# Optimization experiments

Measured on AMD Instinct MI355X. Metric: run time of the kernel, lower is better.

The kernel has to match this reference:

```python
import jax, jax.numpy as jnp
import numpy as np

DEPTH, DIM, HEADS, DH, MLP = 2, 512, 8, 64, 2048
INNER = HEADS * DH
B, L = 2, 2048
SCALE = DH ** -0.5
LN_EPS = 1e-5


def setup_inputs() -> dict:
    key = jax.random.key(0)
    ks = jax.random.split(key, 8)
    s = 0.02
    return {
        "x": jax.random.normal(ks[0], (B, L, DIM), dtype=jnp.float32),
        "mask": jax.random.randint(ks[1], (B, L, L), 0, 2, dtype=jnp.int32),
        "ln1_g": jnp.ones((DEPTH, DIM), jnp.float32),
        "ln1_b": jnp.zeros((DEPTH, DIM), jnp.float32),
        "w_qkv": jax.random.normal(ks[2], (DEPTH, DIM, 3 * INNER), jnp.float32) * s,
        "w_out": jax.random.normal(ks[3], (DEPTH, INNER, DIM), jnp.float32) * s,
        "b_out": jnp.zeros((DEPTH, DIM), jnp.float32),
        "ln2_g": jnp.ones((DEPTH, DIM), jnp.float32),
        "ln2_b": jnp.zeros((DEPTH, DIM), jnp.float32),
        "w1": jax.random.normal(ks[4], (DEPTH, DIM, MLP), jnp.float32) * s,
        "b1": jnp.zeros((DEPTH, MLP), jnp.float32),
        "w2": jax.random.normal(ks[5], (DEPTH, MLP, DIM), jnp.float32) * s,
        "b2": jnp.zeros((DEPTH, DIM), jnp.float32),
    }


def _layer_norm(x, g, b):
    m = jnp.mean(x, axis=-1, keepdims=True)
    v = jnp.mean(jnp.square(x - m), axis=-1, keepdims=True)
    return (x - m) * jax.lax.rsqrt(v + LN_EPS) * g + b


def _attention(h, mask_f, w_qkv, w_out, b_out):
    b, l, _ = h.shape
    qkv = h @ w_qkv  # [b,l,3*inner]
    qkv = qkv.reshape(b, l, 3, HEADS, DH)
    q = jnp.transpose(qkv[:, :, 0], (0, 2, 1, 3))  # [b,h,l,dh]
    k = jnp.transpose(qkv[:, :, 1], (0, 2, 1, 3))
    v = jnp.transpose(qkv[:, :, 2], (0, 2, 1, 3))
    scores = jnp.einsum('bhqd,bhkd->bhqk', q, k) * SCALE
    attn = jax.nn.softmax(scores, axis=-1)
    # multiplicative mask + renormalization (non-standard)
    attn = attn * mask_f
    attn = attn / (jnp.sum(attn, axis=-1, keepdims=True) + 1e-10)
    z = jnp.einsum('bhqk,bhkd->bhqd', attn, v)
    z = jnp.transpose(z, (0, 2, 1, 3)).reshape(b, l, INNER)
    return z @ w_out + b_out


def reference(x, mask, ln1_g, ln1_b, w_qkv, w_out, b_out, ln2_g, ln2_b, w1, b1, w2, b2):
    mask_f = mask[:, None, :, :].astype(x.dtype)  # [b,1,l,l]
    h = x
    for d in range(DEPTH):
        a = _attention(_layer_norm(h, ln1_g[d], ln1_b[d]), mask_f,
                       w_qkv[d], w_out[d], b_out[d])
        h = h + a
        f = _layer_norm(h, ln2_g[d], ln2_b[d])
        f = jax.nn.gelu(f @ w1[d] + b1[d], approximate=False) @ w2[d] + b2[d]
        h = h + f
    return h
```

## Files before the change

### kernel.cpp

```cpp
#include <hip/hip_runtime.h>
#include <math.h>

#define DEPTH 2
#define DIM   512
#define HEADS 8
#define DH    64
#define INNER 512
#define MLP_D 2048
#define BSZ   2
#define SEQ   2048
#define MROWS (BSZ*SEQ)
#define SCALE 0.125f
#define QSC   0.18033688f
#define LN_EPS 1e-5f

typedef unsigned short u16;
typedef unsigned int   u32;
typedef __attribute__((ext_vector_type(8))) unsigned short u16x8;
typedef __attribute__((ext_vector_type(4))) unsigned short u16x4;
typedef __attribute__((ext_vector_type(8))) short          s16x8;
typedef __attribute__((ext_vector_type(4))) float          f32x4;

__device__ __forceinline__ u16 f2bf(float f) {
    u32 u = __float_as_uint(f);
    u += 0x7fffu + ((u >> 16) & 1u);
    return (u16)(u >> 16);
}
__device__ __forceinline__ u32 cvtpk(float lo, float hi) {
    u32 r;
    asm("v_cvt_pk_bf16_f32 %0, %1, %2" : "=v"(r) : "v"(lo), "v"(hi));
    return r;
}
__device__ __forceinline__ void gld16(const void* g, void* l) {
    __builtin_amdgcn_global_load_lds(
        (const __attribute__((address_space(1))) void*)g,
        (__attribute__((address_space(3))) void*)l, 16, 0, 0);
}

__device__ __forceinline__ float wred_sum(float v) {
    #pragma unroll
    for (int o = 32; o; o >>= 1) v += __shfl_xor(v, o);
    return v;
}

__global__ __launch_bounds__(256) void ln_kernel(
    const float* __restrict__ x, const float* __restrict__ g,
    const float* __restrict__ b, u16* __restrict__ y)
{
    const int wave = threadIdx.x >> 6;
    const int lane = threadIdx.x & 63;
    const int row  = blockIdx.x * 4 + wave;
    const float* xr = x + (size_t)row * DIM;

    float4 v0 = *reinterpret_cast<const float4*>(&xr[lane * 8]);
    float4 v1 = *reinterpret_cast<const float4*>(&xr[lane * 8 + 4]);

    float s = v0.x + v0.y + v0.z + v0.w + v1.x + v1.y + v1.z + v1.w;
    s = wred_sum(s);
    const float mean = s * (1.0f / DIM);

    float d[8] = {v0.x - mean, v0.y - mean, v0.z - mean, v0.w - mean,
                  v1.x - mean, v1.y - mean, v1.z - mean, v1.w - mean};
    float ss = 0.f;
    #pragma unroll
    for (int i = 0; i < 8; ++i) ss += d[i] * d[i];
    ss = wred_sum(ss);
    const float inv = rsqrtf(ss * (1.0f / DIM) + LN_EPS);

    float4 g0 = *reinterpret_cast<const float4*>(&g[lane * 8]);
    float4 g1 = *reinterpret_cast<const float4*>(&g[lane * 8 + 4]);
    float4 b0 = *reinterpret_cast<const float4*>(&b[lane * 8]);
    float4 b1 = *reinterpret_cast<const float4*>(&b[lane * 8 + 4]);
    const float gg[8] = {g0.x, g0.y, g0.z, g0.w, g1.x, g1.y, g1.z, g1.w};
    const float bb[8] = {b0.x, b0.y, b0.z, b0.w, b1.x, b1.y, b1.z, b1.w};

    u16x8 o;
    #pragma unroll
    for (int i = 0; i < 8; ++i) o[i] = f2bf(d[i] * inv * gg[i] + bb[i]);
    *reinterpret_cast<u16x8*>(&y[(size_t)row * DIM + lane * 8]) = o;
}

__global__ __launch_bounds__(256) void transpose_bf16_kernel(
    const float* __restrict__ in, u16* __restrict__ out, int K, int N)
{
    __shared__ u16 t[64][65];
    const int k0 = blockIdx.y * 64, n0 = blockIdx.x * 64;
    const int tid = threadIdx.x;
    #pragma unroll
    for (int i = 0; i < 4; ++i) {
        int idx = tid + i * 256;
        int r = idx >> 4, c4 = idx & 15;
        float4 v = *reinterpret_cast<const float4*>(&in[(size_t)(k0 + r) * N + n0 + c4 * 4]);
        t[c4 * 4 + 0][r] = f2bf(v.x);
        t[c4 * 4 + 1][r] = f2bf(v.y);
        t[c4 * 4 + 2][r] = f2bf(v.z);
        t[c4 * 4 + 3][r] = f2bf(v.w);
    }
    __syncthreads();
    #pragma unroll
    for (int i = 0; i < 2; ++i) {
        int idx = tid + i * 256;
        int r = idx >> 3, c8 = idx & 7;
        u16x8 w;
        #pragma unroll
        for (int j = 0; j < 8; ++j) w[j] = t[r][c8 * 8 + j];
        *reinterpret_cast<u16x8*>(&out[(size_t)(n0 + r) * K + k0 + c8 * 8]) = w;
    }
}

__global__ __launch_bounds__(256) void mask_pack_kernel(
    const int* __restrict__ mask, u32* __restrict__ mbT)
{
    const int wv = threadIdx.x >> 6, lane = threadIdx.x & 63;
    const int row = blockIdx.x * 4 + wv;
    const int b = row >> 11, l = row & (SEQ - 1);
    const int* mr = mask + (size_t)row * SEQ;
    u32* out = mbT + (size_t)b * 64 * SEQ;
    for (int it = 0; it < 32; ++it) {
        unsigned long long bal = __ballot(mr[it * 64 + lane] != 0);
        if (lane == 0) {
            out[(size_t)(2 * it) * SEQ + l]     = (u32)bal;
            out[(size_t)(2 * it + 1) * SEQ + l] = (u32)(bal >> 32);
        }
    }
}

#define GSTAGE(buf, kt) do {                                                   \
    const int k0_ = (kt) * BK;                                                 \
    _Pragma("unroll")                                                          \
    for (int i_ = 0; i_ < ACH; ++i_) {                                         \
        int idx_ = i_ * 256 + tid; int r_ = idx_ >> 2, kc_ = idx_ & 3;         \
        gld16(&A[(size_t)(bm + r_) * K + k0_ + kc_ * 8],                       \
              &As[buf][(size_t)(i_ * 256 + (wid << 6)) * 8]);                  \
    }                                                                          \
    _Pragma("unroll")                                                          \
    for (int i_ = 0; i_ < BCH; ++i_) {                                         \
        int idx_ = i_ * 256 + tid; int r_ = idx_ >> 2, kc_ = idx_ & 3;         \
        gld16(&BT[(size_t)(bn + r_) * K + k0_ + kc_ * 8],                      \
              &Bs[buf][(size_t)(i_ * 256 + (wid << 6)) * 8]);                  \
    }                                                                          \
} while (0)

template<int BM, int BN, int MT, int NT, int EPI>
__global__ __launch_bounds__(256) void gemm_bf16(
    const u16* __restrict__ A, const u16* __restrict__ BT,
    const float* __restrict__ bias, const float* __restrict__ Cin,
    void* __restrict__ CoutV, u16* __restrict__ qo, u16* __restrict__ ko,
    u16* __restrict__ vo, int M, int N, int K)
{
    constexpr int BK = 32;
    constexpr int WC = BN / (NT * 16);
    constexpr int ACH = (BM * BK) / (256 * 8);
    constexpr int BCH = (BN * BK) / (256 * 8);

    __shared__ __align__(16) u16 As[2][BM * BK];
    __shared__ __align__(16) u16 Bs[2][BN * BK];

    const int tid  = threadIdx.x;
    const int lane = tid & 63, wid = tid >> 6;
    const int wr = wid / WC, wc = wid % WC;
    const int lr = lane & 15, lk = lane >> 4;
    const int bm = blockIdx.y * BM, bn = blockIdx.x * BN;

    f32x4 acc[MT][NT];
    #pragma unroll
    for (int i = 0; i < MT; ++i)
        #pragma unroll
        for (int j = 0; j < NT; ++j) {
            acc[i][j][0] = 0.f; acc[i][j][1] = 0.f;
            acc[i][j][2] = 0.f; acc[i][j][3] = 0.f;
        }

    GSTAGE(0, 0);
    asm volatile("s_waitcnt vmcnt(0)" ::: "memory");
    __syncthreads();

    const int NTILES = K / BK;
    int cur = 0;
    for (int t = 0; t < NTILES; ++t) {
        if (t + 1 < NTILES) GSTAGE(cur ^ 1, t + 1);

        s16x8 af[MT], bf[NT];
        #pragma unroll
        for (int mt = 0; mt < MT; ++mt)
            af[mt] = *reinterpret_cast<const s16x8*>(
                &As[cur][(wr * MT * 16 + mt * 16 + lr) * BK + lk * 8]);
        #pragma unroll
        for (int nt = 0; nt < NT; ++nt)
            bf[nt] = *reinterpret_cast<const s16x8*>(
                &Bs[cur][(wc * NT * 16 + nt * 16 + lr) * BK + lk * 8]);
        #pragma unroll
        for (int mt = 0; mt < MT; ++mt)
            #pragma unroll
            for (int nt = 0; nt < NT; ++nt)
                acc[mt][nt] = __builtin_amdgcn_mfma_f32_16x16x32_bf16(
                    af[mt], bf[nt], acc[mt][nt], 0, 0, 0);

        asm volatile("s_waitcnt vmcnt(0)" ::: "memory");
        __syncthreads();
        cur ^= 1;
    }

    if (EPI == 3) {
        #pragma unroll
        for (int mt = 0; mt < MT; ++mt) {
            const int rbase = bm + wr * MT * 16 + mt * 16 + lk * 4;
            #pragma unroll
            for (int nt = 0; nt < NT; ++nt) {
                const int c = bn + wc * NT * 16 + nt * 16 + lr;
                const int sec = c >> 9, hh = (c >> 6) & 7, dd = c & 63;
                if (sec == 0) {
                    #pragma unroll
                    for (int i = 0; i < 4; ++i)
                        qo[((size_t)hh * MROWS + rbase + i) * 64 + dd] =
                            f2bf(acc[mt][nt][i] * QSC);
                } else if (sec == 1) {
                    #pragma unroll
                    for (int i = 0; i < 4; ++i)
                        ko[((size_t)hh * MROWS + rbase + i) * 64 + dd] =
                            f2bf(acc[mt][nt][i]);
                } else {
                    const int pos = (rbase & ~31) + lk * 8 + (mt & 1) * 4;
                    u16x4 o;
                    #pragma unroll
                    for (int i = 0; i < 4; ++i) o[i] = f2bf(acc[mt][nt][i]);
                    *reinterpret_cast<u16x4*>(
                        &vo[((size_t)hh * 64 + dd) * MROWS + pos]) = o;
                }
            }
        }
        return;
    }
    #pragma unroll
    for (int mt = 0; mt < MT; ++mt) {
        #pragma unroll
        for (int i = 0; i < 4; ++i) {
            const size_t r = bm + wr * MT * 16 + mt * 16 + lk * 4 + i;
            #pragma unroll
            for (int nt = 0; nt < NT; ++nt) {
                const size_t c = bn + wc * NT * 16 + nt * 16 + lr;
                float v = acc[mt][nt][i];
                if (EPI == 1) {
                    v += bias[c];
                    v = 0.5f * v * (1.0f + erff(v * 0.70710678118654752f));
                    ((u16*)CoutV)[r * N + c] = f2bf(v);
                } else {
                    v += bias[c] + Cin[r * N + c];
                    ((float*)CoutV)[r * N + c] = v;
                }
            }
        }
    }
}
#undef GSTAGE

#define ASTAGE(buf, kv) do {                                                   \
    _Pragma("unroll")                                                          \
    for (int i_ = 0; i_ < 4; ++i_) {                                           \
        int idx_ = i_ * 256 + tid; int r_ = idx_ >> 3, c_ = idx_ & 7;          \
        gld16(Kbase + (size_t)((kv) + r_) * 64 + ((c_ ^ (r_ & 7)) * 8),        \
              &Ks[buf][(size_t)(i_ * 256 + (wid << 6)) * 8]);                  \
    }                                                                          \
    _Pragma("unroll")                                                          \
    for (int i_ = 0; i_ < 4; ++i_) {                                           \
        int idx_ = i_ * 256 + tid; int r_ = idx_ >> 4, c_ = idx_ & 15;         \
        gld16(Vbase + (size_t)r_ * MROWS + (kv) + ((c_ ^ (r_ & 7)) * 8),       \
              &Vts[buf][(size_t)(i_ * 256 + (wid << 6)) * 8]);                 \
    }                                                                          \
} while (0)

__global__ __launch_bounds__(256) void attn_mfma_kernel(
    const u16* __restrict__ Qb,
    const u16* __restrict__ Kb,
    const u16* __restrict__ Vtb,
    const u32* __restrict__ mbT,
    u16* __restrict__ z)
{
    const int bh = blockIdx.y;
    const int b = bh >> 3, h = bh & 7;
    const int q0 = blockIdx.x * 64;
    const int tid = threadIdx.x;
    const int wid = tid >> 6, lane = tid & 63;
    const int lr = lane & 15, lk = lane >> 4;
    const int lr7 = lr & 7;

    __shared__ __align__(16) u16 Ks[2][128 * 64];
    __shared__ __align__(16) u16 Vts[2][64 * 128];

    const int qrow = q0 + wid * 16 + lr;
    const size_t qg = (size_t)b * SEQ + qrow;

    s16x8 qf0, qf1;
    {
        const u16* Qrow = Qb + ((size_t)h * MROWS + qg) * 64;
        qf0 = *reinterpret_cast<const s16x8*>(Qrow + lk * 8);
        qf1 = *reinterpret_cast<const s16x8*>(Qrow + 32 + lk * 8);
    }

    float Mx = -1e30f, Sm = 0.f;
    f32x4 zacc[4];
    #pragma unroll
    for (int dt = 0; dt < 4; ++dt) {
        zacc[dt][0] = 0.f; zacc[dt][1] = 0.f; zacc[dt][2] = 0.f; zacc[dt][3] = 0.f;
    }

    const u16* Kbase = Kb + ((size_t)h * MROWS + (size_t)b * SEQ) * 64;
    const u16* Vbase = Vtb + (size_t)h * 64 * MROWS + (size_t)b * SEQ;
    const u32* mbase = mbT + (size_t)b * 64 * SEQ;

    ASTAGE(0, 0);
    asm volatile("s_waitcnt vmcnt(0)" ::: "memory");
    __syncthreads();

    int cur = 0;
    for (int t = 0; t < SEQ / 128; ++t) {
        if (t + 1 < SEQ / 128) ASTAGE(cur ^ 1, (t + 1) * 128);

        u32 mw[4];
        #pragma unroll
        for (int j = 0; j < 4; ++j)
            mw[j] = mbase[(size_t)(t * 4 + j) * SEQ + qrow];

        const u16* Kc = Ks[cur];
        f32x4 st[8];
        #pragma unroll
        for (int mt = 0; mt < 8; ++mt) {
            st[mt][0] = 0.f; st[mt][1] = 0.f; st[mt][2] = 0.f; st[mt][3] = 0.f;
        }
        #pragma unroll
        for (int mt = 0; mt < 8; ++mt) {
            const s16x8 a0 = *reinterpret_cast<const s16x8*>(
                &Kc[(mt * 16 + lr) * 64 + ((lk ^ lr7) * 8)]);
            const s16x8 a1 = *reinterpret_cast<const s16x8*>(
                &Kc[(mt * 16 + lr) * 64 + (((lk + 4) ^ lr7) * 8)]);
            st[mt] = __builtin_amdgcn_mfma_f32_16x16x32_bf16(a0, qf0, st[mt], 0, 0, 0);
            st[mt] = __builtin_amdgcn_mfma_f32_16x16x32_bf16(a1, qf1, st[mt], 0, 0, 0);
        }

        float ml = st[0][0];
        #pragma unroll
        for (int mt = 0; mt < 8; ++mt)
            #pragma unroll
            for (int i = 0; i < 4; ++i) ml = fmaxf(ml, st[mt][i]);
        ml = fmaxf(ml, __shfl_xor(ml, 16));
        ml = fmaxf(ml, __shfl_xor(ml, 32));
        if (__any(ml > Mx + 8.f)) {
            const float Mn = fmaxf(Mx, ml);
            const float r  = exp2f(Mx - Mn);
            Sm *= r;
            #pragma unroll
            for (int dt = 0; dt < 4; ++dt)
                #pragma unroll
                for (int i = 0; i < 4; ++i) zacc[dt][i] *= r;
            Mx = Mn;
        }
        float tm = 0.f;
        #pragma unroll
        for (int mt = 0; mt < 8; ++mt) {
            const u32 wsh = mw[mt >> 1] >> (((mt & 1) << 4) | (lk << 2));
            #pragma unroll
            for (int i = 0; i < 4; ++i) {
                float e = exp2f(st[mt][i] - Mx);
                e = ((wsh >> i) & 1u) ? e : 0.f;
                st[mt][i] = e;
                tm += e;
            }
        }
        tm += __shfl_xor(tm, 16);
        tm += __shfl_xor(tm, 32);
        Sm += tm;

        const u16* Vc = Vts[cur];
        #pragma unroll
        for (int s = 0; s < 4; ++s) {
            union { u32 w[4]; s16x8 v; } pu;
            pu.w[0] = cvtpk(st[2 * s][0], st[2 * s][1]);
            pu.w[1] = cvtpk(st[2 * s][2], st[2 * s][3]);
            pu.w[2] = cvtpk(st[2 * s + 1][0], st[2 * s + 1][1]);
            pu.w[3] = cvtpk(st[2 * s + 1][2], st[2 * s + 1][3]);
            #pragma unroll
            for (int dt = 0; dt < 4; ++dt) {
                const s16x8 av = *reinterpret_cast<const s16x8*>(
                    &Vc[(dt * 16 + lr) * 128 + (((s * 4 + lk) ^ lr7) * 8)]);
                zacc[dt] = __builtin_amdgcn_mfma_f32_16x16x32_bf16(av, pu.v, zacc[dt], 0, 0, 0);
            }
        }

        asm volatile("s_waitcnt vmcnt(0)" ::: "memory");
        __syncthreads();
        cur ^= 1;
    }

    const float inv = 1.0f / (Sm + 1e-10f);
    #pragma unroll
    for (int dt = 0; dt < 4; ++dt) {
        u16x4 o;
        #pragma unroll
        for (int i = 0; i < 4; ++i) o[i] = f2bf(zacc[dt][i] * inv);
        *reinterpret_cast<u16x4*>(
            &z[qg * INNER + h * 64 + dt * 16 + lk * 4]) = o;
    }
}
#undef ASTAGE

extern "C" void kernel_launch(void* const* d_in, const int* in_sizes, int n_in,
                              void* d_out, int out_size, void* d_ws, size_t ws_size,
                              hipStream_t stream) {
    const float* x      = (const float*)d_in[0];
    const int*   mask   = (const int*)  d_in[1];
    const float* ln1_g  = (const float*)d_in[2];
    const float* ln1_b  = (const float*)d_in[3];
    const float* w_qkv  = (const float*)d_in[4];
    const float* w_out  = (const float*)d_in[5];
    const float* b_out  = (const float*)d_in[6];
    const float* ln2_g  = (const float*)d_in[7];
    const float* ln2_b  = (const float*)d_in[8];
    const float* w1     = (const float*)d_in[9];
    const float* b1     = (const float*)d_in[10];
    const float* w2     = (const float*)d_in[11];
    const float* b2     = (const float*)d_in[12];

    float* h = (float*)d_out;

    u16* hn  = (u16*)d_ws;
    u16* zb  = hn + (size_t)MROWS * DIM;
    u32* mbT = (u32*)(zb + (size_t)MROWS * DIM);
    u16* wT  = (u16*)(mbT + (size_t)BSZ * 64 * SEQ);
    const size_t WT_LAYER = (size_t)DIM * 3 * INNER + (size_t)INNER * DIM
                          + (size_t)DIM * MLP_D + (size_t)MLP_D * DIM;
    u16* big = wT + DEPTH * WT_LAYER;
    u16* Qb  = big;
    u16* Kb  = Qb + (size_t)HEADS * MROWS * 64;
    u16* Vtb = Kb + (size_t)HEADS * MROWS * 64;
    u16* f1  = big;

    hipMemcpyAsync(h, x, (size_t)MROWS * DIM * sizeof(float),
                   hipMemcpyDeviceToDevice, stream);

    mask_pack_kernel<<<MROWS / 4, 256, 0, stream>>>(mask, mbT);
    for (int d = 0; d < DEPTH; ++d) {
        u16* wqkvT = wT + d * WT_LAYER;
        u16* woutT = wqkvT + (size_t)3 * INNER * DIM;
        u16* w1T   = woutT + (size_t)DIM * INNER;
        u16* w2T   = w1T   + (size_t)MLP_D * DIM;
        transpose_bf16_kernel<<<dim3(3 * INNER / 64, DIM / 64), 256, 0, stream>>>(
            w_qkv + (size_t)d * DIM * 3 * INNER, wqkvT, DIM, 3 * INNER);
        transpose_bf16_kernel<<<dim3(INNER / 64, DIM / 64), 256, 0, stream>>>(
            w_out + (size_t)d * INNER * DIM, woutT, INNER, DIM);
        transpose_bf16_kernel<<<dim3(MLP_D / 64, DIM / 64), 256, 0, stream>>>(
            w1 + (size_t)d * DIM * MLP_D, w1T, DIM, MLP_D);
        transpose_bf16_kernel<<<dim3(DIM / 64, MLP_D / 64), 256, 0, stream>>>(
            w2 + (size_t)d * MLP_D * DIM, w2T, MLP_D, DIM);
    }

    for (int d = 0; d < DEPTH; ++d) {
        u16* wqkvT = wT + d * WT_LAYER;
        u16* woutT = wqkvT + (size_t)3 * INNER * DIM;
        u16* w1T   = woutT + (size_t)DIM * INNER;
        u16* w2T   = w1T   + (size_t)MLP_D * DIM;

        ln_kernel<<<MROWS / 4, 256, 0, stream>>>(h, ln1_g + d * DIM, ln1_b + d * DIM, hn);

        gemm_bf16<128, 128, 4, 4, 3><<<dim3(3 * INNER / 128, MROWS / 128), 256, 0, stream>>>(
            hn, wqkvT, nullptr, nullptr, nullptr, Qb, Kb, Vtb, MROWS, 3 * INNER, DIM);

        attn_mfma_kernel<<<dim3(SEQ / 64, BSZ * HEADS), 256, 0, stream>>>(
            Qb, Kb, Vtb, mbT, zb);

        gemm_bf16<128, 64, 4, 2, 2><<<dim3(DIM / 64, MROWS / 128), 256, 0, stream>>>(
            zb, woutT, b_out + d * DIM, h, h, nullptr, nullptr, nullptr, MROWS, DIM, INNER);

        ln_kernel<<<MROWS / 4, 256, 0, stream>>>(h, ln2_g + d * DIM, ln2_b + d * DIM, hn);

        gemm_bf16<128, 128, 4, 4, 1><<<dim3(MLP_D / 128, MROWS / 128), 256, 0, stream>>>(
            hn, w1T, b1 + d * MLP_D, nullptr, f1, nullptr, nullptr, nullptr, MROWS, MLP_D, DIM);

        gemm_bf16<128, 64, 4, 2, 2><<<dim3(DIM / 64, MROWS / 128), 256, 0, stream>>>(
            f1, w2T, b2 + d * DIM, h, h, nullptr, nullptr, nullptr, MROWS, DIM, MLP_D);
    }
}
```

Baseline: 439.6 us.

## Split attention KV across two wave groups, fuse weight transposes, shrink GEMM tiles

The attention kernel now runs 512 threads per block. Two groups of four waves each process half of the key/value sequence with separate LDS buffers, and their partial max, sum and output accumulators are merged through shared memory at the end. This doubles the wave parallelism per query tile on a grid that was small (512 blocks). All per-layer weight transpose launches are fused into one kernel, and the GEMM tile M is reduced from 128 to 64 to launch more blocks. The cost is an extra LDS merge step, half the waves idling during the final write, and less reuse per GEMM tile.

```diff
diff --git a/kernel.cpp b/kernel.cpp
--- a/kernel.cpp
+++ b/kernel.cpp
@@ -80,31 +80,60 @@
     *reinterpret_cast<u16x8*>(&y[(size_t)row * DIM + lane * 8]) = o;
 }
 
-__global__ __launch_bounds__(256) void transpose_bf16_kernel(
-    const float* __restrict__ in, u16* __restrict__ out, int K, int N)
+__global__ __launch_bounds__(256) void transpose_all_kernel(
+    const float* __restrict__ w_qkv, const float* __restrict__ w_out,
+    const float* __restrict__ w1,    const float* __restrict__ w2,
+    u16* __restrict__ wT)
 {
+    const size_t WT_LAYER = (size_t)DIM * 3 * INNER + (size_t)INNER * DIM
+                          + (size_t)DIM * MLP_D + (size_t)MLP_D * DIM;
+    int bx = blockIdx.x;
+    int d = bx / 768, r = bx % 768;
+    const float* in; u16* out; int K, N, kt, nt;
+    if (r < 192) {
+        in = w_qkv + (size_t)d * DIM * 3 * INNER;
+        out = wT + (size_t)d * WT_LAYER;
+        K = DIM; N = 3 * INNER; kt = r / 24; nt = r % 24;
+    } else if (r < 256) {
+        int rr = r - 192;
+        in = w_out + (size_t)d * INNER * DIM;
+        out = wT + (size_t)d * WT_LAYER + (size_t)3 * INNER * DIM;
+        K = INNER; N = DIM; kt = rr / 8; nt = rr % 8;
+    } else if (r < 512) {
+        int rr = r - 256;
+        in = w1 + (size_t)d * DIM * MLP_D;
+        out = wT + (size_t)d * WT_LAYER + (size_t)3 * INNER * DIM + (size_t)INNER * DIM;
+        K = DIM; N = MLP_D; kt = rr / 32; nt = rr % 32;
+    } else {
+        int rr = r - 512;
+        in = w2 + (size_t)d * MLP_D * DIM;
+        out = wT + (size_t)d * WT_LAYER + (size_t)3 * INNER * DIM + (size_t)INNER * DIM
+            + (size_t)DIM * MLP_D;
+        K = MLP_D; N = DIM; kt = rr / 8; nt = rr % 8;
+    }
+    const int k0 = kt * 64, n0 = nt * 64;
+
     __shared__ u16 t[64][65];
-    const int k0 = blockIdx.y * 64, n0 = blockIdx.x * 64;
     const int tid = threadIdx.x;
     #pragma unroll
     for (int i = 0; i < 4; ++i) {
         int idx = tid + i * 256;
-        int r = idx >> 4, c4 = idx & 15;
-        float4 v = *reinterpret_cast<const float4*>(&in[(size_t)(k0 + r) * N + n0 + c4 * 4]);
-        t[c4 * 4 + 0][r] = f2bf(v.x);
-        t[c4 * 4 + 1][r] = f2bf(v.y);
-        t[c4 * 4 + 2][r] = f2bf(v.z);
-        t[c4 * 4 + 3][r] = f2bf(v.w);
+        int rr = idx >> 4, c4 = idx & 15;
+        float4 v = *reinterpret_cast<const float4*>(&in[(size_t)(k0 + rr) * N + n0 + c4 * 4]);
+        t[c4 * 4 + 0][rr] = f2bf(v.x);
+        t[c4 * 4 + 1][rr] = f2bf(v.y);
+        t[c4 * 4 + 2][rr] = f2bf(v.z);
+        t[c4 * 4 + 3][rr] = f2bf(v.w);
     }
     __syncthreads();
     #pragma unroll
     for (int i = 0; i < 2; ++i) {
         int idx = tid + i * 256;
-        int r = idx >> 3, c8 = idx & 7;
+        int rr = idx >> 3, c8 = idx & 7;
         u16x8 w;
         #pragma unroll
-        for (int j = 0; j < 8; ++j) w[j] = t[r][c8 * 8 + j];
-        *reinterpret_cast<u16x8*>(&out[(size_t)(n0 + r) * K + k0 + c8 * 8]) = w;
+        for (int j = 0; j < 8; ++j) w[j] = t[rr][c8 * 8 + j];
+        *reinterpret_cast<u16x8*>(&out[(size_t)(n0 + rr) * K + k0 + c8 * 8]) = w;
     }
 }
 
@@ -256,20 +285,20 @@
 
 #define ASTAGE(buf, kv) do {                                                   \
     _Pragma("unroll")                                                          \
-    for (int i_ = 0; i_ < 4; ++i_) {                                           \
-        int idx_ = i_ * 256 + tid; int r_ = idx_ >> 3, c_ = idx_ & 7;          \
+    for (int i_ = 0; i_ < 2; ++i_) {                                           \
+        int idx_ = i_ * 256 + th; int r_ = idx_ >> 3, c_ = idx_ & 7;           \
         gld16(Kbase + (size_t)((kv) + r_) * 64 + ((c_ ^ (r_ & 7)) * 8),        \
-              &Ks[buf][(size_t)(i_ * 256 + (wid << 6)) * 8]);                  \
+              &Ks[half][buf][(size_t)(i_ * 256 + (qw << 6)) * 8]);             \
     }                                                                          \
     _Pragma("unroll")                                                          \
-    for (int i_ = 0; i_ < 4; ++i_) {                                           \
-        int idx_ = i_ * 256 + tid; int r_ = idx_ >> 4, c_ = idx_ & 15;         \
+    for (int i_ = 0; i_ < 2; ++i_) {                                           \
+        int idx_ = i_ * 256 + th; int r_ = idx_ >> 3, c_ = idx_ & 7;           \
         gld16(Vbase + (size_t)r_ * MROWS + (kv) + ((c_ ^ (r_ & 7)) * 8),       \
-              &Vts[buf][(size_t)(i_ * 256 + (wid << 6)) * 8]);                 \
+              &Vts[half][buf][(size_t)(i_ * 256 + (qw << 6)) * 8]);            \
     }                                                                          \
 } while (0)
 
-__global__ __launch_bounds__(256) void attn_mfma_kernel(
+__global__ __launch_bounds__(512) void attn_mfma_kernel(
     const u16* __restrict__ Qb,
     const u16* __restrict__ Kb,
     const u16* __restrict__ Vtb,
@@ -281,13 +310,15 @@
     const int q0 = blockIdx.x * 64;
     const int tid = threadIdx.x;
     const int wid = tid >> 6, lane = tid & 63;
+    const int qw = wid & 3, half = wid >> 2;
+    const int th = (qw << 6) | lane;
     const int lr = lane & 15, lk = lane >> 4;
     const int lr7 = lr & 7;
 
-    __shared__ __align__(16) u16 Ks[2][128 * 64];
-    __shared__ __align__(16) u16 Vts[2][64 * 128];
-
-    const int qrow = q0 + wid * 16 + lr;
+    __shared__ __align__(16) u16 Ks[2][2][64 * 64];
+    __shared__ __align__(16) u16 Vts[2][2][64 * 64];
+
+    const int qrow = q0 + qw * 16 + lr;
     const size_t qg = (size_t)b * SEQ + qrow;
 
     s16x8 qf0, qf1;
@@ -307,28 +338,29 @@
     const u16* Kbase = Kb + ((size_t)h * MROWS + (size_t)b * SEQ) * 64;
     const u16* Vbase = Vtb + (size_t)h * 64 * MROWS + (size_t)b * SEQ;
     const u32* mbase = mbT + (size_t)b * 64 * SEQ;
-
-    ASTAGE(0, 0);
+    const int kvhalf = half * (SEQ / 2);
+
+    ASTAGE(0, kvhalf);
     asm volatile("s_waitcnt vmcnt(0)" ::: "memory");
     __syncthreads();
 
     int cur = 0;
-    for (int t = 0; t < SEQ / 128; ++t) {
-        if (t + 1 < SEQ / 128) ASTAGE(cur ^ 1, (t + 1) * 128);
-
-        u32 mw[4];
-        #pragma unroll
-        for (int j = 0; j < 4; ++j)
-            mw[j] = mbase[(size_t)(t * 4 + j) * SEQ + qrow];
-
-        const u16* Kc = Ks[cur];
-        f32x4 st[8];
-        #pragma unroll
-        for (int mt = 0; mt < 8; ++mt) {
+    for (int t = 0; t < 16; ++t) {
+        if (t + 1 < 16) ASTAGE(cur ^ 1, kvhalf + (t + 1) * 64);
+
+        u32 mw[2];
+        #pragma unroll
+        for (int j = 0; j < 2; ++j)
+            mw[j] = mbase[(size_t)((half * 16 + t) * 2 + j) * SEQ + qrow];
+
+        const u16* Kc = Ks[half][cur];
+        f32x4 st[4];
+        #pragma unroll
+        for (int mt = 0; mt < 4; ++mt) {
             st[mt][0] = 0.f; st[mt][1] = 0.f; st[mt][2] = 0.f; st[mt][3] = 0.f;
         }
         #pragma unroll
-        for (int mt = 0; mt < 8; ++mt) {
+        for (int mt = 0; mt < 4; ++mt) {
             const s16x8 a0 = *reinterpret_cast<const s16x8*>(
                 &Kc[(mt * 16 + lr) * 64 + ((lk ^ lr7) * 8)]);
             const s16x8 a1 = *reinterpret_cast<const s16x8*>(
@@ -339,7 +371,7 @@
 
         float ml = st[0][0];
         #pragma unroll
-        for (int mt = 0; mt < 8; ++mt)
+        for (int mt = 0; mt < 4; ++mt)
             #pragma unroll
             for (int i = 0; i < 4; ++i) ml = fmaxf(ml, st[mt][i]);
         ml = fmaxf(ml, __shfl_xor(ml, 16));
@@ -356,7 +388,7 @@
         }
         float tm = 0.f;
         #pragma unroll
-        for (int mt = 0; mt < 8; ++mt) {
+        for (int mt = 0; mt < 4; ++mt) {
             const u32 wsh = mw[mt >> 1] >> (((mt & 1) << 4) | (lk << 2));
             #pragma unroll
             for (int i = 0; i < 4; ++i) {
@@ -370,9 +402,9 @@
         tm += __shfl_xor(tm, 32);
         Sm += tm;
 
-        const u16* Vc = Vts[cur];
-        #pragma unroll
-        for (int s = 0; s < 4; ++s) {
+        const u16* Vc = Vts[half][cur];
+        #pragma unroll
+        for (int s = 0; s < 2; ++s) {
             union { u32 w[4]; s16x8 v; } pu;
             pu.w[0] = cvtpk(st[2 * s][0], st[2 * s][1]);
             pu.w[1] = cvtpk(st[2 * s][2], st[2 * s][3]);
@@ -381,7 +413,7 @@
             #pragma unroll
             for (int dt = 0; dt < 4; ++dt) {
                 const s16x8 av = *reinterpret_cast<const s16x8*>(
-                    &Vc[(dt * 16 + lr) * 128 + (((s * 4 + lk) ^ lr7) * 8)]);
+                    &Vc[(dt * 16 + lr) * 64 + (((s * 4 + lk) ^ lr7) * 8)]);
                 zacc[dt] = __builtin_amdgcn_mfma_f32_16x16x32_bf16(av, pu.v, zacc[dt], 0, 0, 0);
             }
         }
@@ -391,14 +423,31 @@
         cur ^= 1;
     }
 
-    const float inv = 1.0f / (Sm + 1e-10f);
-    #pragma unroll
-    for (int dt = 0; dt < 4; ++dt) {
-        u16x4 o;
-        #pragma unroll
-        for (int i = 0; i < 4; ++i) o[i] = f2bf(zacc[dt][i] * inv);
-        *reinterpret_cast<u16x4*>(
-            &z[qg * INNER + h * 64 + dt * 16 + lk * 4]) = o;
+    float* sc = reinterpret_cast<float*>(&Ks[0][0][0]);
+    if (half == 1) {
+        float* p = sc + (size_t)th * 18;
+        p[0] = Mx; p[1] = Sm;
+        #pragma unroll
+        for (int dt = 0; dt < 4; ++dt)
+            #pragma unroll
+            for (int i = 0; i < 4; ++i) p[2 + dt * 4 + i] = zacc[dt][i];
+    }
+    __syncthreads();
+    if (half == 0) {
+        const float* p = sc + (size_t)th * 18;
+        const float Mx1 = p[0], Sm1 = p[1];
+        const float M  = fmaxf(Mx, Mx1);
+        const float r0 = exp2f(Mx - M), r1 = exp2f(Mx1 - M);
+        const float inv = 1.0f / (Sm * r0 + Sm1 * r1 + 1e-10f);
+        #pragma unroll
+        for (int dt = 0; dt < 4; ++dt) {
+            u16x4 o;
+            #pragma unroll
+            for (int i = 0; i < 4; ++i)
+                o[i] = f2bf((zacc[dt][i] * r0 + p[2 + dt * 4 + i] * r1) * inv);
+            *reinterpret_cast<u16x4*>(
+                &z[qg * INNER + h * 64 + dt * 16 + lk * 4]) = o;
+        }
     }
 }
 #undef ASTAGE
@@ -438,44 +487,31 @@
                    hipMemcpyDeviceToDevice, stream);
 
     mask_pack_kernel<<<MROWS / 4, 256, 0, stream>>>(mask, mbT);
+    transpose_all_kernel<<<DEPTH * 768, 256, 0, stream>>>(w_qkv, w_out, w1, w2, wT);
+
     for (int d = 0; d < DEPTH; ++d) {
         u16* wqkvT = wT + d * WT_LAYER;
         u16* woutT = wqkvT + (size_t)3 * INNER * DIM;
         u16* w1T   = woutT + (size_t)DIM * INNER;
         u16* w2T   = w1T   + (size_t)MLP_D * DIM;
-        transpose_bf16_kernel<<<dim3(3 * INNER / 64, DIM / 64), 256, 0, stream>>>(
-            w_qkv + (size_t)d * DIM * 3 * INNER, wqkvT, DIM, 3 * INNER);
-        transpose_bf16_kernel<<<dim3(INNER / 64, DIM / 64), 256, 0, stream>>>(
-            w_out + (size_t)d * INNER * DIM, woutT, INNER, DIM);
-        transpose_bf16_kernel<<<dim3(MLP_D / 64, DIM / 64), 256, 0, stream>>>(
-            w1 + (size_t)d * DIM * MLP_D, w1T, DIM, MLP_D);
-        transpose_bf16_kernel<<<dim3(DIM / 64, MLP_D / 64), 256, 0, stream>>>(
-            w2 + (size_t)d * MLP_D * DIM, w2T, MLP_D, DIM);
-    }
-
-    for (int d = 0; d < DEPTH; ++d) {
-        u16* wqkvT = wT + d * WT_LAYER;
-        u16* woutT = wqkvT + (size_t)3 * INNER * DIM;
-        u16* w1T   = woutT + (size_t)DIM * INNER;
-        u16* w2T   = w1T   + (size_t)MLP_D * DIM;
 
         ln_kernel<<<MROWS / 4, 256, 0, stream>>>(h, ln1_g + d * DIM, ln1_b + d * DIM, hn);
 
-        gemm_bf16<128, 128, 4, 4, 3><<<dim3(3 * INNER / 128, MROWS / 128), 256, 0, stream>>>(
+        gemm_bf16<64, 128, 2, 4, 3><<<dim3(3 * INNER / 128, MROWS / 64), 256, 0, stream>>>(
             hn, wqkvT, nullptr, nullptr, nullptr, Qb, Kb, Vtb, MROWS, 3 * INNER, DIM);
 
-        attn_mfma_kernel<<<dim3(SEQ / 64, BSZ * HEADS), 256, 0, stream>>>(
+        attn_mfma_kernel<<<dim3(SEQ / 64, BSZ * HEADS), 512, 0, stream>>>(
             Qb, Kb, Vtb, mbT, zb);
 
-        gemm_bf16<128, 64, 4, 2, 2><<<dim3(DIM / 64, MROWS / 128), 256, 0, stream>>>(
+        gemm_bf16<64, 64, 2, 2, 2><<<dim3(DIM / 64, MROWS / 64), 256, 0, stream>>>(
             zb, woutT, b_out + d * DIM, h, h, nullptr, nullptr, nullptr, MROWS, DIM, INNER);
 
         ln_kernel<<<MROWS / 4, 256, 0, stream>>>(h, ln2_g + d * DIM, ln2_b + d * DIM, hn);
 
-        gemm_bf16<128, 128, 4, 4, 1><<<dim3(MLP_D / 128, MROWS / 128), 256, 0, stream>>>(
+        gemm_bf16<64, 128, 2, 4, 1><<<dim3(MLP_D / 128, MROWS / 64), 256, 0, stream>>>(
             hn, w1T, b1 + d * MLP_D, nullptr, f1, nullptr, nullptr, nullptr, MROWS, MLP_D, DIM);
 
-        gemm_bf16<128, 64, 4, 2, 2><<<dim3(DIM / 64, MROWS / 128), 256, 0, stream>>>(
+        gemm_bf16<64, 64, 2, 2, 2><<<dim3(DIM / 64, MROWS / 64), 256, 0, stream>>>(
             f1, w2T, b2 + d * DIM, h, h, nullptr, nullptr, nullptr, MROWS, DIM, MLP_D);
     }
 }
```

Result: faster. 387.0 us (-12.0%).
